# Kernel tuning notes

Measured on AMD Instinct MI355X. Metric: run time of the kernel, lower is better.

The kernel has to match this reference:

```python
import jax, jax.numpy as jnp
import numpy as np

N, D, TOP_K = 200000, 256, 1024
L = 64
EPS = 1e-8  # matches F.cosine_similarity eps


def setup_inputs() -> dict:
    key = jax.random.key(0)
    k1, k2, k3, k4, k5 = jax.random.split(key, 5)
    return {
        "node_embeddings": jax.random.normal(k1, (N, D), dtype=jnp.float32),
        "dist_table": jax.random.normal(k2, (3, 2), dtype=jnp.float32),       # nn.Embedding(3,2)
        "W": jax.random.normal(k3, (D, D + 2), dtype=jnp.float32) / np.sqrt(D + 2),  # Linear(d+2->d, no bias)
        "distance_tensor": jax.random.randint(k4, (N,), 0, 4),
        "label_node_idx": jax.random.randint(k5, (L,), 0, N),
        "source_node_idx": 12345,
    }


def reference(node_embeddings, dist_table, W, distance_tensor, label_node_idx, source_node_idx):
    # distance encoding lookup: clamp(dist-1, 0, 2)
    d_idx = jnp.clip(distance_tensor.astype(jnp.int32) - 1, 0, 2)
    denc = dist_table[d_idx]                                         # [N, 2]
    x = jnp.concatenate([node_embeddings, denc], axis=1)             # [N, D+2]
    transformed = x @ W.T                                            # [N, D]

    # cosine similarity of source embedding vs all transformed embeddings
    q = node_embeddings[source_node_idx]                             # [D]
    qn = q / jnp.maximum(jnp.linalg.norm(q), EPS)
    tn = transformed / jnp.maximum(
        jnp.linalg.norm(transformed, axis=1, keepdims=True), EPS)
    cos = tn @ qn                                                    # [N]

    # validity mask and distance weights (1.0 / 1.5 / 2.0)
    valid = distance_tensor <= 2
    w = jnp.where(distance_tensor == 1, 1.5,
                  jnp.where(distance_tensor == 2, 2.0, 1.0)).astype(cos.dtype)
    weighted = jnp.where(valid, cos * w, -jnp.inf)                   # invalid -> never selected
    _, topk_idx = jax.lax.top_k(weighted, TOP_K)                     # N_valid >> TOP_K here

    # softmax-style retrieval loss: sum_labels (logsumexp(all.q) - label.q)
    logits = transformed @ q                                         # [N]
    lse = jax.nn.logsumexp(logits)
    loss = jnp.sum(lse - logits[label_node_idx])

    # final_top_k = unique(topk U one-hop U source); fixed-shape boolean membership mask
    mask = jnp.zeros((N,), dtype=bool).at[topk_idx].set(True)
    mask = mask | (distance_tensor == 1) | (jnp.arange(N) == source_node_idx)
    return loss, mask
```

## Files before the change

### kernel.cpp

```cpp
#include <hip/hip_runtime.h>
#include <math.h>

#define D 256
#define TOPK 1024
#define EPS 1e-8f

typedef __attribute__((ext_vector_type(8))) short short8;
typedef __attribute__((ext_vector_type(4))) float f32x4;

__device__ __forceinline__ unsigned encf(float f){
  unsigned b = __float_as_uint(f);
  return b ^ ((unsigned)((int)b >> 31) | 0x80000000u);
}
__device__ __forceinline__ float decf(unsigned u){
  unsigned b = (u & 0x80000000u) ? (u ^ 0x80000000u) : ~u;
  return __uint_as_float(b);
}

__device__ __forceinline__ void gload16(const void* g, void* l){
  __builtin_amdgcn_global_load_lds(
      (const __attribute__((address_space(1))) unsigned*)g,
      (__attribute__((address_space(3))) unsigned*)l, 16, 0, 0);
}

__global__ __launch_bounds__(256) void k1_setup(
    const float* __restrict__ emb, const float* __restrict__ dtab,
    const float* __restrict__ W, const int* __restrict__ srcp,
    short* __restrict__ Wbs, float* __restrict__ WD, float* __restrict__ QN,
    unsigned* __restrict__ SC, unsigned* __restrict__ H0)
{
  int tid = threadIdx.x;
  int gid = blockIdx.x*256 + tid;
  if (gid < 6144) H0[gid] = 0u;
  if (gid == 0){
    SC[0]=0u;
    ((float*)SC)[1]=0.0f;
    SC[2]=0u;
    SC[3]=0u;
    SC[4]=(unsigned)TOPK;
  }
  if (blockIdx.x < 256){
    int c = blockIdx.x;
    int k = tid;
    float f = W[(size_t)c*258 + k];
    unsigned u  = __float_as_uint(f);
    unsigned hb = u & 0xffff0000u;
    float r = f - __uint_as_float(hb);
    unsigned mb = __float_as_uint(r) & 0xffff0000u;
    float r2 = r - __uint_as_float(mb);
    unsigned lb = __float_as_uint(r2) & 0xffff0000u;
    int ch = k >> 5, kk = k & 31;
    Wbs[((size_t)(ch*3+0)*256 + c)*40 + kk] = (short)(hb>>16);
    Wbs[((size_t)(ch*3+1)*256 + c)*40 + kk] = (short)(mb>>16);
    Wbs[((size_t)(ch*3+2)*256 + c)*40 + kk] = (short)(lb>>16);
  } else {
    int k = tid;
    float w6 = W[(size_t)k*258 + 256], w7 = W[(size_t)k*258 + 257];
    WD[k]     = w6*dtab[0] + w7*dtab[1];
    WD[256+k] = w6*dtab[2] + w7*dtab[3];
    WD[512+k] = w6*dtab[4] + w7*dtab[5];
    int src = srcp[0];
    float qk = emb[(size_t)src*D + k];
    __shared__ float red[256];
    red[tid]=qk*qk; __syncthreads();
    for (int s2=128;s2>0;s2>>=1){ if (tid<s2) red[tid]+=red[tid+s2]; __syncthreads(); }
    if (tid==0) QN[0] = sqrtf(red[0]);
  }
}

#define SPLIT(x0,x1, AH,AM,AL) do{ float xs[8]={x0.x,x0.y,x0.z,x0.w,x1.x,x1.y,x1.z,x1.w}; \
  _Pragma("unroll") for(int _e=0;_e<8;++_e){ float _f=xs[_e]; unsigned _u=__float_as_uint(_f); \
    unsigned _hb=_u&0xffff0000u; float _r=_f-__uint_as_float(_hb); \
    unsigned _mb=__float_as_uint(_r)&0xffff0000u; float _r2=_r-__uint_as_float(_mb); \
    unsigned _lb=__float_as_uint(_r2)&0xffff0000u; \
    AH[_e]=(short)(_hb>>16); AM[_e]=(short)(_mb>>16); AL[_e]=(short)(_lb>>16);} }while(0)

#define STAGE(bufi, st) do{ if (tid < 256){ \
  const char* _s = (const char*)Wbs + (size_t)(st)*20480; \
  char* _d = (char*)&bst[bufi][0]; \
  _Pragma("unroll") for (int _i=0;_i<5;++_i){ int _o=(_i*256+tid)*16; gload16(_s+_o, _d+_o);} } }while(0)

#define READB(bufi) do{ const short* _bp = &bst[bufi][0] + rdoff; \
  _Pragma("unroll") for (int _bf=0;_bf<8;++_bf) b[_bf] = *(const short8*)(_bp + _bf*640); }while(0)

#define PASS(A0_, A1_) do{ _Pragma("unroll") for (int _bf=0;_bf<8;++_bf){ \
  acc0[_bf] = __builtin_amdgcn_mfma_f32_16x16x32_bf16(A0_, b[_bf], acc0[_bf],0,0,0); \
  acc1[_bf] = __builtin_amdgcn_mfma_f32_16x16x32_bf16(A1_, b[_bf], acc1[_bf],0,0,0); } }while(0)

__global__ __launch_bounds__(512,2) void k2_main(
    const float* __restrict__ emb, const int* __restrict__ dist,
    const int* __restrict__ srcp, const short* __restrict__ Wbs,
    const float* __restrict__ WD, const float* __restrict__ QN,
    float* __restrict__ Sv, unsigned* __restrict__ UK,
    unsigned* __restrict__ SC, unsigned* __restrict__ H0, int N)
{
  int tid = threadIdx.x;
  int wave = tid >> 6;
  int lane = tid & 63;
  int g = lane >> 4;
  int c0 = lane & 15;
  int rs = wave >> 1;
  int cH = wave & 1;
  int blockbase = blockIdx.x*128;

  __shared__ short bst[2][10240];
  __shared__ float wdL[3][256];
  __shared__ float qL[256];
  __shared__ float QS[2][128][2];
  __shared__ int   dL[128];
  __shared__ unsigned h[2048];

  STAGE(0, 0);
  for (int i=tid;i<768;i+=512) ((float*)wdL)[i] = WD[i];
  if (tid < 256) qL[tid] = emb[(size_t)srcp[0]*D + tid];
  if (tid < 128){ int rr = blockbase + tid; dL[tid] = (rr<N)? dist[rr] : 3; }
  for (int i=tid;i<2048;i+=512) h[i]=0u;

  int r0 = blockbase + rs*32 + c0;
  int r1 = r0 + 16;
  const float* xp0 = emb + (size_t)(r0<N? r0 : (N-1))*D + 8*g;
  const float* xp1 = emb + (size_t)(r1<N? r1 : (N-1))*D + 8*g;

  float4 xA0 = *(const float4*)(xp0);
  float4 xA1 = *(const float4*)(xp0+4);
  float4 xB0 = *(const float4*)(xp1);
  float4 xB1 = *(const float4*)(xp1+4);
  float4 nA0,nA1,nB0,nB1;

  f32x4 acc0[8], acc1[8];
  #pragma unroll
  for (int f=0;f<8;++f){ acc0[f]=(f32x4){0.f,0.f,0.f,0.f}; acc1[f]=(f32x4){0.f,0.f,0.f,0.f}; }

  int rdoff = (cH*128 + c0)*40 + g*8;
  short8 b[8];
  short8 ah0,am0,al0,ah1,am1,al1;

  __syncthreads();

  for (int ch=0; ch<8; ++ch){
    int bufA = ch & 1;
    SPLIT(xA0,xA1, ah0,am0,al0);
    SPLIT(xB0,xB1, ah1,am1,al1);
    if (ch < 7){
      nA0 = *(const float4*)(xp0 + 32*(ch+1));
      nA1 = *(const float4*)(xp0 + 32*(ch+1) + 4);
      nB0 = *(const float4*)(xp1 + 32*(ch+1));
      nB1 = *(const float4*)(xp1 + 32*(ch+1) + 4);
    }
    STAGE(bufA^1, 3*ch+1);
    READB(bufA);
    PASS(ah0, ah1);
    PASS(am0, am1);
    PASS(al0, al1);
    __syncthreads();
    STAGE(bufA, 3*ch+2);
    READB(bufA^1);
    PASS(ah0, ah1);
    PASS(am0, am1);
    __syncthreads();
    if (ch < 7) STAGE(bufA^1, 3*ch+3);
    READB(bufA);
    PASS(ah0, ah1);
    if (ch < 7){ xA0=nA0; xA1=nA1; xB0=nB0; xB1=nB1; }
    __syncthreads();
  }

  #pragma unroll
  for (int af=0; af<2; ++af){
    #pragma unroll
    for (int r=0;r<4;++r){
      int rl = rs*32 + af*16 + 4*g + r;
      int dv = dL[rl];
      int di = dv-1; di = di<0?0:(di>2?2:di);
      float S=0.f, Q=0.f;
      #pragma unroll
      for (int bf=0;bf<8;++bf){
        int col = cH*128 + 16*bf + c0;
        float v = (af ? acc1[bf][r] : acc0[bf][r]) + wdL[di][col];
        S = fmaf(v, qL[col], S);
        Q = fmaf(v, v, Q);
      }
      #pragma unroll
      for (int off=1; off<16; off<<=1){ S += __shfl_xor(S,off); Q += __shfl_xor(Q,off); }
      if (c0==0){ QS[cH][rl][0]=S; QS[cH][rl][1]=Q; }
    }
  }
  __syncthreads();

  float sred = -INFINITY;
  if (tid < 128){
    int row = blockbase + tid;
    if (row < N){
      float S = QS[0][tid][0] + QS[1][tid][0];
      float Q = QS[0][tid][1] + QS[1][tid][1];
      int dv = dL[tid];
      float qn = QN[0];
      float den = fmaxf(sqrtf(Q), EPS) * fmaxf(qn, EPS);
      float cosv = S/den;
      float wgt = (dv==1)?1.5f:((dv==2)?2.0f:1.0f);
      float wv = (dv<=2)? cosv*wgt : -INFINITY;
      unsigned u = encf(wv);
      Sv[row]=S; UK[row]=u;
      if (u > 0x007FFFFFu) atomicAdd(&h[u>>21],1u);
      sred = S;
    }
  }
  if (wave < 2){
    float m = sred;
    #pragma unroll
    for (int off=32;off>0;off>>=1) m = fmaxf(m, __shfl_down(m,off));
    if (lane==0) atomicMax(&SC[0], encf(m));
  }
  __syncthreads();
  for (int i=tid;i<2048;i+=512){ unsigned v=h[i]; if (v) atomicAdd(&H0[i], v); }
}

__global__ __launch_bounds__(256) void kh_hist(
    const unsigned* __restrict__ UK, const unsigned* __restrict__ SC,
    unsigned* __restrict__ Hp, int pass, int N)
{
  __shared__ unsigned h[2048];
  int bins = (pass==2)?1024:2048;
  int tid = threadIdx.x;
  for (int i=tid;i<bins;i+=256) h[i]=0u;
  __syncthreads();
  unsigned pfx = SC[3];
  int n = blockIdx.x*256 + tid;
  if (n < N){
    unsigned u = UK[n];
    bool incl; unsigned bin;
    if (pass==1){ incl = ((u>>21)==pfx); bin = (u>>10)&2047u; }
    else { incl = ((u>>10)==pfx); bin = u & 1023u; }
    if (incl) atomicAdd(&h[bin], 1u);
  }
  __syncthreads();
  for (int i=tid;i<bins;i+=256){ unsigned v=h[i]; if (v) atomicAdd(&Hp[i], v); }
}

__global__ __launch_bounds__(256) void ks_scan(
    const unsigned* __restrict__ Hp, unsigned* __restrict__ SC, int pass)
{
  __shared__ unsigned h[2048];
  __shared__ unsigned part[256];
  int bins=(pass==2)?1024:2048;
  int per = bins/256;
  int tid=threadIdx.x;
  unsigned ps=0;
  for (int i=0;i<per;++i){ unsigned v=Hp[tid*per+i]; h[tid*per+i]=v; ps+=v; }
  part[tid]=ps;
  __syncthreads();
  if (tid==0){
    unsigned Kp = SC[4];
    unsigned cum=0;
    int sc2=0;
    for (int t=255;t>=0;--t){
      if (cum + part[t] >= Kp){ sc2=t; break; }
      cum += part[t];
    }
    int sel = sc2*per;
    for (int b2=sc2*per+per-1; b2>=sc2*per; --b2){
      if (cum + h[b2] >= Kp){ sel=b2; break; }
      cum += h[b2];
    }
    SC[4] = Kp - cum;
    int bitsp = (pass==2)?10:11;
    SC[3] = (SC[3] << bitsp) | (unsigned)sel;
  }
}

__global__ __launch_bounds__(256) void k6_final(
    const int* __restrict__ dist, const int* __restrict__ srcp,
    const float* __restrict__ Sv, const unsigned* __restrict__ UK,
    unsigned* __restrict__ SC, unsigned* __restrict__ EQL,
    float* __restrict__ out, int N)
{
  int tid=threadIdx.x;
  int n=blockIdx.x*256+tid;
  unsigned T = SC[3];
  float M = decf(SC[0]);
  int src = srcp[0];
  float e=0.f;
  if (n<N){
    unsigned u = UK[n];
    int dv = dist[n];
    bool base = (u>T) || (dv==1) || (n==src);
    out[1+n] = base ? 1.0f : 0.0f;
    if (u==T){
      unsigned i = atomicAdd(&SC[2], 1u);
      if (i < 4096u) EQL[i] = (unsigned)n;
    }
    e = expf(Sv[n]-M);
  }
  __shared__ float red[256];
  red[tid]=e; __syncthreads();
  for (int st=128;st>0;st>>=1){ if (tid<st) red[tid]+=red[tid+st]; __syncthreads(); }
  if (tid==0) atomicAdd((float*)&SC[1], red[0]);
}

__global__ __launch_bounds__(256) void k7_loss(
    const int* __restrict__ labels, const float* __restrict__ Sv,
    unsigned* __restrict__ SC, const unsigned* __restrict__ EQL,
    float* __restrict__ out, int L)
{
  __shared__ float red[256];
  __shared__ unsigned lst[4096];
  int tid=threadIdx.x;
  float v=0.f;
  if (tid<L) v = Sv[labels[tid]];
  red[tid]=v; __syncthreads();
  for (int st=128;st>0;st>>=1){ if (tid<st) red[tid]+=red[tid+st]; __syncthreads(); }
  if (tid==0){
    float M = decf(SC[0]);
    float se = ((const float*)SC)[1];
    out[0] = (float)L*(M + logf(se)) - red[0];
  }
  unsigned cnt = SC[2]; if (cnt>4096u) cnt=4096u;
  unsigned quota = SC[4];
  for (unsigned i=tid;i<cnt;i+=256u) lst[i]=EQL[i];
  __syncthreads();
  if (cnt <= quota){
    for (unsigned i=tid;i<cnt;i+=256u) out[1+lst[i]] = 1.0f;
  } else {
    for (unsigned i=tid;i<cnt;i+=256u){
      unsigned me=lst[i]; unsigned rank=0;
      for (unsigned j=0;j<cnt;++j) rank += (lst[j]<me)?1u:0u;
      if (rank<quota) out[1+me]=1.0f;
    }
  }
}

extern "C" void kernel_launch(void* const* d_in, const int* in_sizes, int n_in,
                              void* d_out, int out_size, void* d_ws, size_t ws_size,
                              hipStream_t stream)
{
  const float* emb  = (const float*)d_in[0];
  const float* dtab = (const float*)d_in[1];
  const float* W    = (const float*)d_in[2];
  const int* dist   = (const int*)d_in[3];
  const int* labels = (const int*)d_in[4];
  const int* srcp   = (const int*)d_in[5];
  float* out = (float*)d_out;
  int N = in_sizes[3];
  int L = in_sizes[4];

  float* ws = (float*)d_ws;
  short* Wbs = (short*)ws;
  float* WD  = (float*)(Wbs + 245760);
  float* QN  = WD + 768;
  unsigned* SC = (unsigned*)(QN + 1);
  unsigned* H0 = SC + 8;
  unsigned* H1 = H0 + 2048;
  unsigned* H2 = H1 + 2048;
  float* Sv = (float*)(H2 + 2048);
  unsigned* UK = (unsigned*)(Sv + N);
  unsigned* EQL = UK + N;

  int grid  = (N + 255)/256;
  int gridm = (N + 127)/128;
  k1_setup<<<257,256,0,stream>>>(emb, dtab, W, srcp, Wbs, WD, QN, SC, H0);
  k2_main<<<gridm,512,0,stream>>>(emb, dist, srcp, Wbs, WD, QN, Sv, UK, SC, H0, N);
  ks_scan<<<1,256,0,stream>>>(H0, SC, 0);
  kh_hist<<<grid,256,0,stream>>>(UK, SC, H1, 1, N);
  ks_scan<<<1,256,0,stream>>>(H1, SC, 1);
  kh_hist<<<grid,256,0,stream>>>(UK, SC, H2, 2, N);
  ks_scan<<<1,256,0,stream>>>(H2, SC, 2);
  k6_final<<<grid,256,0,stream>>>(dist, srcp, Sv, UK, SC, EQL, out, N);
  k7_loss<<<1,256,0,stream>>>(labels, Sv, SC, EQL, out, L);
}
```

Baseline: 502.5 us.

## Persistent GEMM with column-quarter W resident in LDS and atomic row reductions

The main kernel becomes a persistent grid of 256 blocks. Each block holds a quarter of the split-bf16 weight matrix (64 columns) resident in 96KB of dynamic LDS and streams a contiguous row range, so the per-chunk W staging and barriers go away. Partial dot products and squared norms per row are combined across the four column quarters with float atomics into zero-initialized global arrays. A new encode kernel then computes the cosine keys, histogram and max. In exchange, each embedding row is read four times (once per column quarter), the run adds global atomics and an extra launch, and atomic ordering makes the floating-point sums nondeterministic.

```diff
diff --git a/kernel.cpp b/kernel.cpp
--- a/kernel.cpp
+++ b/kernel.cpp
@@ -27,20 +27,19 @@
     const float* __restrict__ emb, const float* __restrict__ dtab,
     const float* __restrict__ W, const int* __restrict__ srcp,
     short* __restrict__ Wbs, float* __restrict__ WD, float* __restrict__ QN,
-    unsigned* __restrict__ SC, unsigned* __restrict__ H0)
+    unsigned* __restrict__ SC, unsigned* __restrict__ ZB, int N)
 {
   int tid = threadIdx.x;
-  int gid = blockIdx.x*256 + tid;
-  if (gid < 6144) H0[gid] = 0u;
-  if (gid == 0){
+  int blk = blockIdx.x;
+  if (blk == 0 && tid == 0){
     SC[0]=0u;
     ((float*)SC)[1]=0.0f;
     SC[2]=0u;
     SC[3]=0u;
     SC[4]=(unsigned)TOPK;
   }
-  if (blockIdx.x < 256){
-    int c = blockIdx.x;
+  if (blk < 256){
+    int c = blk;
     int k = tid;
     float f = W[(size_t)c*258 + k];
     unsigned u  = __float_as_uint(f);
@@ -49,11 +48,13 @@
     unsigned mb = __float_as_uint(r) & 0xffff0000u;
     float r2 = r - __uint_as_float(mb);
     unsigned lb = __float_as_uint(r2) & 0xffff0000u;
-    int ch = k >> 5, kk = k & 31;
-    Wbs[((size_t)(ch*3+0)*256 + c)*40 + kk] = (short)(hb>>16);
-    Wbs[((size_t)(ch*3+1)*256 + c)*40 + kk] = (short)(mb>>16);
-    Wbs[((size_t)(ch*3+2)*256 + c)*40 + kk] = (short)(lb>>16);
-  } else {
+    int q = c >> 6, colq = c & 63, cf = colq >> 4, c0 = colq & 15;
+    int ch = k >> 5, kk = k & 31, g = kk >> 3, e = kk & 7;
+    size_t idx0 = (size_t)q*49152 + ((size_t)(ch*3)*4 + cf)*512 + (g*16 + c0)*8 + e;
+    Wbs[idx0       ] = (short)(hb>>16);
+    Wbs[idx0 + 2048] = (short)(mb>>16);
+    Wbs[idx0 + 4096] = (short)(lb>>16);
+  } else if (blk == 256){
     int k = tid;
     float w6 = W[(size_t)k*258 + 256], w7 = W[(size_t)k*258 + 257];
     WD[k]     = w6*dtab[0] + w7*dtab[1];
@@ -65,6 +66,9 @@
     red[tid]=qk*qk; __syncthreads();
     for (int s2=128;s2>0;s2>>=1){ if (tid<s2) red[tid]+=red[tid+s2]; __syncthreads(); }
     if (tid==0) QN[0] = sqrtf(red[0]);
+  } else {
+    unsigned zid = (unsigned)(blk-257)*256u + (unsigned)tid;
+    if (zid < 6144u + 2u*(unsigned)N) ZB[zid] = 0u;
   }
 }
 
@@ -75,144 +79,167 @@
     unsigned _lb=__float_as_uint(_r2)&0xffff0000u; \
     AH[_e]=(short)(_hb>>16); AM[_e]=(short)(_mb>>16); AL[_e]=(short)(_lb>>16);} }while(0)
 
-#define STAGE(bufi, st) do{ if (tid < 256){ \
-  const char* _s = (const char*)Wbs + (size_t)(st)*20480; \
-  char* _d = (char*)&bst[bufi][0]; \
-  _Pragma("unroll") for (int _i=0;_i<5;++_i){ int _o=(_i*256+tid)*16; gload16(_s+_o, _d+_o);} } }while(0)
-
-#define READB(bufi) do{ const short* _bp = &bst[bufi][0] + rdoff; \
-  _Pragma("unroll") for (int _bf=0;_bf<8;++_bf) b[_bf] = *(const short8*)(_bp + _bf*640); }while(0)
-
-#define PASS(A0_, A1_) do{ _Pragma("unroll") for (int _bf=0;_bf<8;++_bf){ \
-  acc0[_bf] = __builtin_amdgcn_mfma_f32_16x16x32_bf16(A0_, b[_bf], acc0[_bf],0,0,0); \
-  acc1[_bf] = __builtin_amdgcn_mfma_f32_16x16x32_bf16(A1_, b[_bf], acc1[_bf],0,0,0); } }while(0)
+#define READB(S_) do{ _Pragma("unroll") for (int _cf=0;_cf<4;++_cf) \
+  b[_cf] = *(const short8*)(Bsh + ((ch*3+(S_))*4+_cf)*512 + (lane<<3)); }while(0)
+
+#define MFMA_PASS(ASPL) do{ _Pragma("unroll") for (int _rf=0;_rf<4;++_rf){ \
+  _Pragma("unroll") for (int _cf=0;_cf<4;++_cf) \
+    acc[_rf][_cf] = __builtin_amdgcn_mfma_f32_16x16x32_bf16(ASPL[_rf], b[_cf], acc[_rf][_cf],0,0,0); } }while(0)
 
 __global__ __launch_bounds__(512,2) void k2_main(
     const float* __restrict__ emb, const int* __restrict__ dist,
     const int* __restrict__ srcp, const short* __restrict__ Wbs,
-    const float* __restrict__ WD, const float* __restrict__ QN,
-    float* __restrict__ Sv, unsigned* __restrict__ UK,
-    unsigned* __restrict__ SC, unsigned* __restrict__ H0, int N)
-{
+    const float* __restrict__ WD, float* __restrict__ Sg,
+    float* __restrict__ Qg, int N)
+{
+  extern __shared__ short Bsh[];
   int tid = threadIdx.x;
   int wave = tid >> 6;
   int lane = tid & 63;
   int g = lane >> 4;
   int c0 = lane & 15;
-  int rs = wave >> 1;
-  int cH = wave & 1;
-  int blockbase = blockIdx.x*128;
-
-  __shared__ short bst[2][10240];
-  __shared__ float wdL[3][256];
-  __shared__ float qL[256];
-  __shared__ float QS[2][128][2];
-  __shared__ int   dL[128];
+
+  int q  = blockIdx.x & 3;
+  int rb = blockIdx.x >> 2;
+  int RPB = (N + 63) >> 6;
+  int rstart = rb * RPB;
+  int rend = rstart + RPB; if (rend > N) rend = N;
+  int ITERS = (RPB + 511) >> 9;
+
+  const char* Wq = (const char*)(Wbs + (size_t)q*49152);
+  #pragma unroll
+  for (int i=0;i<12;++i){
+    int off = (i*512 + tid)*16;
+    gload16(Wq + off, (char*)Bsh + off);
+  }
+
+  int colbase = q*64;
+  float qq[4], wdq0[4], wdq1[4], wdq2[4];
+  {
+    int src = srcp[0];
+    #pragma unroll
+    for (int cf=0;cf<4;++cf){
+      int col = colbase + cf*16 + c0;
+      qq[cf]   = emb[(size_t)src*D + col];
+      wdq0[cf] = WD[col];
+      wdq1[cf] = WD[256+col];
+      wdq2[cf] = WD[512+col];
+    }
+  }
+  __syncthreads();
+
+  for (int it=0; it<ITERS; ++it){
+    int rowbase = rstart + it*512 + wave*64;
+    const float* xp0; const float* xp1; const float* xp2; const float* xp3;
+    {
+      int r0 = rowbase + c0;        xp0 = emb + (size_t)(r0<N? r0 : N-1)*D + 8*g;
+      int r1 = rowbase + 16 + c0;   xp1 = emb + (size_t)(r1<N? r1 : N-1)*D + 8*g;
+      int r2 = rowbase + 32 + c0;   xp2 = emb + (size_t)(r2<N? r2 : N-1)*D + 8*g;
+      int r3 = rowbase + 48 + c0;   xp3 = emb + (size_t)(r3<N? r3 : N-1)*D + 8*g;
+    }
+    f32x4 acc[4][4];
+    #pragma unroll
+    for (int rf=0;rf<4;++rf)
+      #pragma unroll
+      for (int cf=0;cf<4;++cf) acc[rf][cf] = (f32x4){0.f,0.f,0.f,0.f};
+
+    float4 xc[4][2], xn[4][2];
+    xc[0][0]=*(const float4*)(xp0); xc[0][1]=*(const float4*)(xp0+4);
+    xc[1][0]=*(const float4*)(xp1); xc[1][1]=*(const float4*)(xp1+4);
+    xc[2][0]=*(const float4*)(xp2); xc[2][1]=*(const float4*)(xp2+4);
+    xc[3][0]=*(const float4*)(xp3); xc[3][1]=*(const float4*)(xp3+4);
+
+    for (int ch=0; ch<8; ++ch){
+      if (ch < 7){
+        int o = 32*(ch+1);
+        xn[0][0]=*(const float4*)(xp0+o); xn[0][1]=*(const float4*)(xp0+o+4);
+        xn[1][0]=*(const float4*)(xp1+o); xn[1][1]=*(const float4*)(xp1+o+4);
+        xn[2][0]=*(const float4*)(xp2+o); xn[2][1]=*(const float4*)(xp2+o+4);
+        xn[3][0]=*(const float4*)(xp3+o); xn[3][1]=*(const float4*)(xp3+o+4);
+      }
+      short8 ah[4], am[4], al[4];
+      #pragma unroll
+      for (int rf=0;rf<4;++rf) SPLIT(xc[rf][0], xc[rf][1], ah[rf], am[rf], al[rf]);
+
+      short8 b[4];
+      READB(0);
+      MFMA_PASS(ah);
+      MFMA_PASS(am);
+      MFMA_PASS(al);
+      READB(1);
+      MFMA_PASS(ah);
+      MFMA_PASS(am);
+      READB(2);
+      MFMA_PASS(ah);
+
+      if (ch < 7){
+        #pragma unroll
+        for (int rf=0;rf<4;++rf){ xc[rf][0]=xn[rf][0]; xc[rf][1]=xn[rf][1]; }
+      }
+    }
+
+    #pragma unroll
+    for (int rf=0; rf<4; ++rf){
+      #pragma unroll
+      for (int r=0;r<4;++r){
+        int row = rowbase + rf*16 + 4*g + r;
+        bool wr = (row < rend);
+        int dv = wr ? dist[row] : 3;
+        int di = dv-1; di = di<0?0:(di>2?2:di);
+        float S=0.f, Q=0.f;
+        #pragma unroll
+        for (int cf=0;cf<4;++cf){
+          float wd = (di==0)? wdq0[cf] : (di==1)? wdq1[cf] : wdq2[cf];
+          float v = acc[rf][cf][r] + wd;
+          S = fmaf(v, qq[cf], S);
+          Q = fmaf(v, v, Q);
+        }
+        #pragma unroll
+        for (int off=1; off<16; off<<=1){
+          S += __shfl_xor(S, off);
+          Q += __shfl_xor(Q, off);
+        }
+        if (c0==0 && wr){
+          atomicAdd(&Sg[row], S);
+          atomicAdd(&Qg[row], Q);
+        }
+      }
+    }
+  }
+}
+
+__global__ __launch_bounds__(256) void k2b_enc(
+    const int* __restrict__ dist, const float* __restrict__ Sg,
+    const float* __restrict__ Qg, const float* __restrict__ QN,
+    unsigned* __restrict__ UK, unsigned* __restrict__ SC,
+    unsigned* __restrict__ H0, int N)
+{
   __shared__ unsigned h[2048];
-
-  STAGE(0, 0);
-  for (int i=tid;i<768;i+=512) ((float*)wdL)[i] = WD[i];
-  if (tid < 256) qL[tid] = emb[(size_t)srcp[0]*D + tid];
-  if (tid < 128){ int rr = blockbase + tid; dL[tid] = (rr<N)? dist[rr] : 3; }
-  for (int i=tid;i<2048;i+=512) h[i]=0u;
-
-  int r0 = blockbase + rs*32 + c0;
-  int r1 = r0 + 16;
-  const float* xp0 = emb + (size_t)(r0<N? r0 : (N-1))*D + 8*g;
-  const float* xp1 = emb + (size_t)(r1<N? r1 : (N-1))*D + 8*g;
-
-  float4 xA0 = *(const float4*)(xp0);
-  float4 xA1 = *(const float4*)(xp0+4);
-  float4 xB0 = *(const float4*)(xp1);
-  float4 xB1 = *(const float4*)(xp1+4);
-  float4 nA0,nA1,nB0,nB1;
-
-  f32x4 acc0[8], acc1[8];
+  int tid = threadIdx.x;
+  int lane = tid & 63;
+  for (int i=tid;i<2048;i+=256) h[i]=0u;
+  __syncthreads();
+  int n = blockIdx.x*256 + tid;
+  float sval = -INFINITY;
+  if (n < N){
+    float S = Sg[n], Q = Qg[n];
+    int dv = dist[n];
+    float qn = QN[0];
+    float den = fmaxf(sqrtf(Q), EPS) * fmaxf(qn, EPS);
+    float cosv = S/den;
+    float wgt = (dv==1)?1.5f:((dv==2)?2.0f:1.0f);
+    float wv = (dv<=2)? cosv*wgt : -INFINITY;
+    unsigned u = encf(wv);
+    UK[n] = u;
+    if (u > 0x007FFFFFu) atomicAdd(&h[u>>21],1u);
+    sval = S;
+  }
+  float m = sval;
   #pragma unroll
-  for (int f=0;f<8;++f){ acc0[f]=(f32x4){0.f,0.f,0.f,0.f}; acc1[f]=(f32x4){0.f,0.f,0.f,0.f}; }
-
-  int rdoff = (cH*128 + c0)*40 + g*8;
-  short8 b[8];
-  short8 ah0,am0,al0,ah1,am1,al1;
-
-  __syncthreads();
-
-  for (int ch=0; ch<8; ++ch){
-    int bufA = ch & 1;
-    SPLIT(xA0,xA1, ah0,am0,al0);
-    SPLIT(xB0,xB1, ah1,am1,al1);
-    if (ch < 7){
-      nA0 = *(const float4*)(xp0 + 32*(ch+1));
-      nA1 = *(const float4*)(xp0 + 32*(ch+1) + 4);
-      nB0 = *(const float4*)(xp1 + 32*(ch+1));
-      nB1 = *(const float4*)(xp1 + 32*(ch+1) + 4);
-    }
-    STAGE(bufA^1, 3*ch+1);
-    READB(bufA);
-    PASS(ah0, ah1);
-    PASS(am0, am1);
-    PASS(al0, al1);
-    __syncthreads();
-    STAGE(bufA, 3*ch+2);
-    READB(bufA^1);
-    PASS(ah0, ah1);
-    PASS(am0, am1);
-    __syncthreads();
-    if (ch < 7) STAGE(bufA^1, 3*ch+3);
-    READB(bufA);
-    PASS(ah0, ah1);
-    if (ch < 7){ xA0=nA0; xA1=nA1; xB0=nB0; xB1=nB1; }
-    __syncthreads();
-  }
-
-  #pragma unroll
-  for (int af=0; af<2; ++af){
-    #pragma unroll
-    for (int r=0;r<4;++r){
-      int rl = rs*32 + af*16 + 4*g + r;
-      int dv = dL[rl];
-      int di = dv-1; di = di<0?0:(di>2?2:di);
-      float S=0.f, Q=0.f;
-      #pragma unroll
-      for (int bf=0;bf<8;++bf){
-        int col = cH*128 + 16*bf + c0;
-        float v = (af ? acc1[bf][r] : acc0[bf][r]) + wdL[di][col];
-        S = fmaf(v, qL[col], S);
-        Q = fmaf(v, v, Q);
-      }
-      #pragma unroll
-      for (int off=1; off<16; off<<=1){ S += __shfl_xor(S,off); Q += __shfl_xor(Q,off); }
-      if (c0==0){ QS[cH][rl][0]=S; QS[cH][rl][1]=Q; }
-    }
-  }
-  __syncthreads();
-
-  float sred = -INFINITY;
-  if (tid < 128){
-    int row = blockbase + tid;
-    if (row < N){
-      float S = QS[0][tid][0] + QS[1][tid][0];
-      float Q = QS[0][tid][1] + QS[1][tid][1];
-      int dv = dL[tid];
-      float qn = QN[0];
-      float den = fmaxf(sqrtf(Q), EPS) * fmaxf(qn, EPS);
-      float cosv = S/den;
-      float wgt = (dv==1)?1.5f:((dv==2)?2.0f:1.0f);
-      float wv = (dv<=2)? cosv*wgt : -INFINITY;
-      unsigned u = encf(wv);
-      Sv[row]=S; UK[row]=u;
-      if (u > 0x007FFFFFu) atomicAdd(&h[u>>21],1u);
-      sred = S;
-    }
-  }
-  if (wave < 2){
-    float m = sred;
-    #pragma unroll
-    for (int off=32;off>0;off>>=1) m = fmaxf(m, __shfl_down(m,off));
-    if (lane==0) atomicMax(&SC[0], encf(m));
-  }
-  __syncthreads();
-  for (int i=tid;i<2048;i+=512){ unsigned v=h[i]; if (v) atomicAdd(&H0[i], v); }
+  for (int off=32;off>0;off>>=1) m = fmaxf(m, __shfl_down(m, off));
+  if (lane==0) atomicMax(&SC[0], encf(m));
+  __syncthreads();
+  for (int i=tid;i<2048;i+=256){ unsigned v=h[i]; if (v) atomicAdd(&H0[i], v); }
 }
 
 __global__ __launch_bounds__(256) void kh_hist(
@@ -345,25 +372,34 @@
 
   float* ws = (float*)d_ws;
   short* Wbs = (short*)ws;
-  float* WD  = (float*)(Wbs + 245760);
+  float* WD  = (float*)(Wbs + 196608);
   float* QN  = WD + 768;
   unsigned* SC = (unsigned*)(QN + 1);
   unsigned* H0 = SC + 8;
   unsigned* H1 = H0 + 2048;
   unsigned* H2 = H1 + 2048;
-  float* Sv = (float*)(H2 + 2048);
-  unsigned* UK = (unsigned*)(Sv + N);
+  float* Sg = (float*)(H2 + 2048);
+  float* Qg = Sg + N;
+  unsigned* UK = (unsigned*)(Qg + N);
   unsigned* EQL = UK + N;
 
+  static bool lds_inited = false;
+  if (!lds_inited){
+    hipFuncSetAttribute((const void*)k2_main,
+                        hipFuncAttributeMaxDynamicSharedMemorySize, 98304);
+    lds_inited = true;
+  }
+
   int grid  = (N + 255)/256;
-  int gridm = (N + 127)/128;
-  k1_setup<<<257,256,0,stream>>>(emb, dtab, W, srcp, Wbs, WD, QN, SC, H0);
-  k2_main<<<gridm,512,0,stream>>>(emb, dist, srcp, Wbs, WD, QN, Sv, UK, SC, H0, N);
+  int grid1 = 257 + (6144 + 2*N + 255)/256;
+  k1_setup<<<grid1,256,0,stream>>>(emb, dtab, W, srcp, Wbs, WD, QN, SC, H0, N);
+  k2_main<<<256,512,98304,stream>>>(emb, dist, srcp, Wbs, WD, Sg, Qg, N);
+  k2b_enc<<<grid,256,0,stream>>>(dist, Sg, Qg, QN, UK, SC, H0, N);
   ks_scan<<<1,256,0,stream>>>(H0, SC, 0);
   kh_hist<<<grid,256,0,stream>>>(UK, SC, H1, 1, N);
   ks_scan<<<1,256,0,stream>>>(H1, SC, 1);
   kh_hist<<<grid,256,0,stream>>>(UK, SC, H2, 2, N);
   ks_scan<<<1,256,0,stream>>>(H2, SC, 2);
-  k6_final<<<grid,256,0,stream>>>(dist, srcp, Sv, UK, SC, EQL, out, N);
-  k7_loss<<<1,256,0,stream>>>(labels, Sv, SC, EQL, out, L);
-}
+  k6_final<<<grid,256,0,stream>>>(dist, srcp, Sg, UK, SC, EQL, out, N);
+  k7_loss<<<1,256,0,stream>>>(labels, Sg, SC, EQL, out, L);
+}
```

After: 507.6 us. About the same (+1.0%).
